# Performance work log

Measured on AMD Instinct MI355X. Metric: run time of the kernel, lower is better.

The kernel has to match this reference:

```python
import jax, jax.numpy as jnp
import numpy as np

B, T, C, H = 4096, 128, 128, 64  # T must equal BLOCK_SIZE=128, C=EMBEDDING_DIM=128


def setup_inputs() -> dict:
    key = jax.random.key(0)
    k1, k2, k3, k4, k5, k6 = jax.random.split(key, 6)
    source_embedding = jax.random.normal(k1, (B, T, C), dtype=jnp.float32)
    target_embedding = jax.random.normal(k2, (B, T, C), dtype=jnp.float32)
    # realistic padding: positions < length are valid; guarantees col 0 valid (no NaN rows)
    lengths = jax.random.randint(k3, (B,), 1, T + 1)
    pad_mask = jnp.arange(T)[None, :] < lengths[:, None]  # (B, T) bool
    Wq = jax.random.normal(k4, (C, H), dtype=jnp.float32) * 0.02
    Wk = jax.random.normal(k5, (C, H), dtype=jnp.float32) * 0.02
    Wv = jax.random.normal(k6, (C, H), dtype=jnp.float32) * 0.02
    return {"source_embedding": source_embedding, "target_embedding": target_embedding,
            "pad_mask": pad_mask, "Wq": Wq, "Wk": Wk, "Wv": Wv}


def reference(source_embedding, target_embedding, pad_mask, Wq, Wk, Wv):
    # q from target, k/v from source (cross-attention capable), bias-free projections
    q = target_embedding @ Wq   # (B, T, H)
    k = source_embedding @ Wk   # (B, T, H)
    v = source_embedding @ Wv   # (B, T, H)
    scale = k.shape[-1] ** -0.5
    wei = jnp.einsum('btd,bsd->bts', q, k) * scale  # (B, T, T)
    causal = jnp.tril(jnp.ones((T, T), dtype=bool))  # needs_future_mask=True
    mask = pad_mask[:, None, :] & causal[None, :, :]  # fuse pad + future masks
    wei = jnp.where(mask, wei, -jnp.inf)
    wei = jax.nn.softmax(wei, axis=-1)
    # dropout disabled (eval mode) for deterministic reference
    out = wei @ v  # (B, T, H)
    return out
```

## Files before the change

### kernel.cpp

```cpp
#include <hip/hip_runtime.h>
#include <stdint.h>


typedef uint32_t u32x2 __attribute__((ext_vector_type(2)));
typedef uint32_t u32x4 __attribute__((ext_vector_type(4)));
typedef float    f32x4 __attribute__((ext_vector_type(4)));
typedef __bf16   bf16x8 __attribute__((ext_vector_type(8)));

static __device__ __forceinline__ uint32_t pack2(float a, float b) {
  uint32_t ua = __builtin_bit_cast(uint32_t, a);
  uint32_t ub = __builtin_bit_cast(uint32_t, b);
  ua += 0x7FFFu + ((ua >> 16) & 1u);
  ub += 0x7FFFu + ((ub >> 16) & 1u);
  return (ua >> 16) | (ub & 0xFFFF0000u);
}
static __device__ __forceinline__ f32x4 mfma16(u32x4 a, u32x4 b, f32x4 c) {
  return __builtin_amdgcn_mfma_f32_16x16x32_bf16(
      __builtin_bit_cast(bf16x8, a), __builtin_bit_cast(bf16x8, b), c, 0, 0, 0);
}

__global__ void prep_w(const float* __restrict__ Wq, const float* __restrict__ Wk,
                       const float* __restrict__ Wv, const void* __restrict__ mask,
                       uint32_t* __restrict__ ws) {
  const int blk = blockIdx.x;
  const int l = threadIdx.x;
  if (blk < 48) {
    const int m  = blk >> 4;
    const int ct = (blk >> 2) & 3;
    const int ks = blk & 3;
    const float* W = (m == 0) ? Wq : ((m == 1) ? Wk : Wv);
    const int h  = ct * 16 + (l & 15);
    const int c0 = ks * 32 + (l >> 4) * 8;
    u32x4 v;
#pragma unroll
    for (int p = 0; p < 4; ++p)
      v[p] = pack2(W[(c0 + 2 * p) * 64 + h], W[(c0 + 2 * p + 1) * 64 + h]);
    ((u32x4*)ws)[blk * 64 + l] = v;
  } else {
    const uint32_t* mw = (const uint32_t*)mask;
    int fl = 0;
    for (int i = l * 16; i < l * 16 + 16; ++i) {
      uint32_t x = mw[i];
      if (x == 0x3F800000u) fl = 2;
      else if (x > 1u && fl != 2) fl = 1;
    }
#pragma unroll
    for (int off = 32; off > 0; off >>= 1) {
      int o = __shfl_down(fl, off);
      fl = (o > fl) ? o : fl;
    }
    if (l == 0) ws[12288] = (uint32_t)fl;
  }
}

__global__ __launch_bounds__(512, 3) void attn_fused(
    const float* __restrict__ src, const float* __restrict__ tgt,
    const void* __restrict__ mask, const uint32_t* __restrict__ ws,
    float* __restrict__ out) {
  __shared__ __align__(16) uint8_t lds[49664];
  uint8_t* const EMB = lds;
  uint8_t* const Kb  = lds + 16384;
  uint8_t* const Vb  = lds + 32768;
  float*  const BIAS = (float*)(lds + 49152);

  const int b   = blockIdx.x;
  const int tid = (int)threadIdx.x;
  const int l   = tid & 63;
  const int w   = tid >> 6;
  const int l15 = l & 15;
  const int g4  = l >> 4;
  const int ct  = w & 3;
  const int sg  = (w >> 2) * 2;

  const u32x4* wsv = (const u32x4*)ws;
  const int mflag = (int)ws[12288];
  const float* const srcb = src + (size_t)b * 16384;
  const float* const tgtb = tgt + (size_t)b * 16384;

  u32x4 wk[4], wv[4];
#pragma unroll
  for (int ks = 0; ks < 4; ++ks) {
    wk[ks] = wsv[((4 + ct) * 4 + ks) * 64 + l];
    wv[ks] = wsv[((8 + ct) * 4 + ks) * 64 + l];
  }

  f32x4 pf[4];
  auto stage_load = [&](const float* gbase) {
#pragma unroll
    for (int p = 0; p < 4; ++p)
      pf[p] = *(const f32x4*)(gbase + tid * 4 + p * 2048);
  };
  auto stage_write = [&]() {
#pragma unroll
    for (int p = 0; p < 4; ++p) {
      const int c   = tid + p * 512;
      const int row = c >> 5;
      const int cc  = c & 31;
      u32x2 d = { pack2(pf[p][0], pf[p][1]), pack2(pf[p][2], pf[p][3]) };
      *(u32x2*)(EMB + (row << 8) + ((((cc >> 1) ^ (row & 7))) << 4) + ((cc & 1) << 3)) = d;
    }
  };

  auto projKV = [&](int half) {
#pragma unroll
    for (int i = 0; i < 2; ++i) {
      const int st  = sg + i;
      const int row = st * 16 + l15;
      f32x4 cK = {0, 0, 0, 0}, cV = {0, 0, 0, 0};
#pragma unroll
      for (int ks = 0; ks < 4; ++ks) {
        u32x4 e = *(const u32x4*)(EMB + (row << 8) + ((((ks * 4 + g4) ^ (row & 7))) << 4));
        cK = mfma16(wk[ks], e, cK);
        cV = mfma16(e, wv[ks], cV);
      }
      const int s  = half * 64 + st * 16 + l15;
      const int h0 = ct * 16 + g4 * 4;
      u32x2 dk = { pack2(cK[0], cK[1]), pack2(cK[2], cK[3]) };
      *(u32x2*)(Kb + (s << 7) + ((((h0 >> 3) ^ (s & 7))) << 4) + ((h0 & 7) << 1)) = dk;
      const int s0 = half * 64 + st * 16 + g4 * 4;
      const int h  = ct * 16 + l15;
      u32x2 dv = { pack2(cV[0], cV[1]), pack2(cV[2], cV[3]) };
      *(u32x2*)(Vb + (h << 8) + ((((s0 >> 3) ^ (h & 7))) << 4) + ((s0 & 7) << 1)) = dv;
    }
  };

  uint32_t qp[8];
  auto projQ_own = [&]() {
    const int row = (w & 3) * 16 + l15;
    f32x4 c0 = {0,0,0,0}, c1 = {0,0,0,0}, c2 = {0,0,0,0}, c3 = {0,0,0,0};
#pragma unroll
    for (int ks = 0; ks < 4; ++ks) {
      u32x4 e = *(const u32x4*)(EMB + (row << 8) + ((((ks * 4 + g4) ^ (row & 7))) << 4));
      c0 = mfma16(wsv[(0  + ks) * 64 + l], e, c0);
      c1 = mfma16(wsv[(4  + ks) * 64 + l], e, c1);
      c2 = mfma16(wsv[(8  + ks) * 64 + l], e, c2);
      c3 = mfma16(wsv[(12 + ks) * 64 + l], e, c3);
    }
    qp[0] = pack2(c0[0], c0[1]); qp[1] = pack2(c0[2], c0[3]);
    qp[2] = pack2(c1[0], c1[1]); qp[3] = pack2(c1[2], c1[3]);
    qp[4] = pack2(c2[0], c2[1]); qp[5] = pack2(c2[2], c2[3]);
    qp[6] = pack2(c3[0], c3[1]); qp[7] = pack2(c3[2], c3[3]);
  };

  stage_load(srcb);
  float biasv = 0.0f;
  if (tid < 128) {
    bool valid;
    if (mflag == 1)      valid = ((const uint8_t*)mask)[b * 128 + tid] != 0;
    else if (mflag == 0) valid = ((const int*)mask)[b * 128 + tid] != 0;
    else                 valid = ((const float*)mask)[b * 128 + tid] != 0.0f;
    biasv = valid ? 0.0f : -1e30f;
  }
  stage_write();
  if (tid < 128) BIAS[tid] = biasv;
  __syncthreads();
  stage_load(srcb + 8192);
  projKV(0);
  __syncthreads();
  stage_write();
  __syncthreads();
  stage_load(tgtb);
  projKV(1);
  __syncthreads();
  stage_write();
  __syncthreads();
  stage_load(tgtb + 8192);
  if (w < 4) projQ_own();
  __syncthreads();
  stage_write();
  __syncthreads();
  if (w >= 4) projQ_own();

  const int hi2 = g4 >> 1;
  const int sA  = ((g4 & 1) * 2) * 16 + l15;
  const int sB  = sA + 16;

  u32x4 qB[2];
#pragma unroll
  for (int ks = 0; ks < 2; ++ks) {
    uint32_t a0 = (uint32_t)__shfl((int)qp[4 * ks + 0], sA);
    uint32_t a1 = (uint32_t)__shfl((int)qp[4 * ks + 1], sA);
    uint32_t a2 = (uint32_t)__shfl((int)qp[4 * ks + 2], sA);
    uint32_t a3 = (uint32_t)__shfl((int)qp[4 * ks + 3], sA);
    uint32_t b0 = (uint32_t)__shfl((int)qp[4 * ks + 0], sB);
    uint32_t b1 = (uint32_t)__shfl((int)qp[4 * ks + 1], sB);
    uint32_t b2 = (uint32_t)__shfl((int)qp[4 * ks + 2], sB);
    uint32_t b3 = (uint32_t)__shfl((int)qp[4 * ks + 3], sB);
    qB[ks][0] = hi2 ? a2 : a0;
    qB[ks][1] = hi2 ? a3 : a1;
    qB[ks][2] = hi2 ? b2 : b0;
    qB[ks][3] = hi2 ? b3 : b1;
  }

  const int tq = 16 * w + l15;
  f32x4 sacc[8];
#pragma unroll
  for (int mt = 0; mt < 8; ++mt) sacc[mt] = {0, 0, 0, 0};
  __builtin_amdgcn_s_setprio(1);
#pragma unroll
  for (int mt = 0; mt < 8; ++mt) {
    const int srow = mt * 16 + l15;
    u32x4 k0 = *(const u32x4*)(Kb + (srow << 7) + (((g4 ^ (srow & 7))) << 4));
    u32x4 k1 = *(const u32x4*)(Kb + (srow << 7) + ((((4 + g4) ^ (srow & 7))) << 4));
    sacc[mt] = mfma16(k0, qB[0], sacc[mt]);
    sacc[mt] = mfma16(k1, qB[1], sacc[mt]);
  }
  __builtin_amdgcn_s_setprio(0);

  float m = -3.0e38f;
#pragma unroll
  for (int mt = 0; mt < 8; ++mt) {
    f32x4 b4 = *(const f32x4*)(BIAS + mt * 16 + g4 * 4);
#pragma unroll
    for (int r = 0; r < 4; ++r) {
      float v = sacc[mt][r] * 0.125f + b4[r];
      sacc[mt][r] = v;
      m = fmaxf(m, v);
    }
  }
  m = fmaxf(m, __shfl_xor(m, 16));
  m = fmaxf(m, __shfl_xor(m, 32));
  float sum = 0.0f;
#pragma unroll
  for (int mt = 0; mt < 8; ++mt) {
#pragma unroll
    for (int r = 0; r < 4; ++r) {
      const int s = mt * 16 + g4 * 4 + r;
      float p = __expf(sacc[mt][r] - m);
      p = (s <= tq) ? p : 0.0f;
      sacc[mt][r] = p;
      sum += p;
    }
  }
  sum += __shfl_xor(sum, 16);
  sum += __shfl_xor(sum, 32);
  const float inv = 1.0f / sum;

  uint32_t sp[16];
#pragma unroll
  for (int mt = 0; mt < 8; ++mt) {
    sp[2 * mt]     = pack2(sacc[mt][0], sacc[mt][1]);
    sp[2 * mt + 1] = pack2(sacc[mt][2], sacc[mt][3]);
  }

  f32x4 oacc[4];
#pragma unroll
  for (int vt = 0; vt < 4; ++vt) oacc[vt] = {0, 0, 0, 0};
  __builtin_amdgcn_s_setprio(1);
#pragma unroll
  for (int ks = 0; ks < 4; ++ks) {
    uint32_t a0 = (uint32_t)__shfl((int)sp[4 * ks + 0], sA);
    uint32_t a1 = (uint32_t)__shfl((int)sp[4 * ks + 1], sA);
    uint32_t a2 = (uint32_t)__shfl((int)sp[4 * ks + 2], sA);
    uint32_t a3 = (uint32_t)__shfl((int)sp[4 * ks + 3], sA);
    uint32_t b0 = (uint32_t)__shfl((int)sp[4 * ks + 0], sB);
    uint32_t b1 = (uint32_t)__shfl((int)sp[4 * ks + 1], sB);
    uint32_t b2 = (uint32_t)__shfl((int)sp[4 * ks + 2], sB);
    uint32_t b3 = (uint32_t)__shfl((int)sp[4 * ks + 3], sB);
    u32x4 pb;
    pb[0] = hi2 ? a2 : a0;
    pb[1] = hi2 ? a3 : a1;
    pb[2] = hi2 ? b2 : b0;
    pb[3] = hi2 ? b3 : b1;
#pragma unroll
    for (int vt = 0; vt < 4; ++vt) {
      const int vrow = vt * 16 + l15;
      u32x4 vf = *(const u32x4*)(Vb + (vrow << 8) + ((((ks * 4 + g4) ^ (vrow & 7))) << 4));
      oacc[vt] = mfma16(vf, pb, oacc[vt]);
    }
  }
  __builtin_amdgcn_s_setprio(0);

  float* const ob = out + (size_t)b * 8192 + (size_t)tq * 64;
#pragma unroll
  for (int vt = 0; vt < 4; ++vt) {
    f32x4 o = { oacc[vt][0] * inv, oacc[vt][1] * inv,
                oacc[vt][2] * inv, oacc[vt][3] * inv };
    *(f32x4*)(ob + vt * 16 + g4 * 4) = o;
  }
}

extern "C" void kernel_launch(void* const* d_in, const int* in_sizes, int n_in,
                              void* d_out, int out_size, void* d_ws, size_t ws_size,
                              hipStream_t stream) {
  const float* src = (const float*)d_in[0];
  const float* tgt = (const float*)d_in[1];
  const void*  msk = d_in[2];
  const float* Wq  = (const float*)d_in[3];
  const float* Wk  = (const float*)d_in[4];
  const float* Wv  = (const float*)d_in[5];
  uint32_t* ws = (uint32_t*)d_ws;
  float* out = (float*)d_out;
  const int B = in_sizes[0] / (128 * 128);

  hipLaunchKernelGGL(prep_w, dim3(49), dim3(64), 0, stream, Wq, Wk, Wv, msk, ws);
  hipLaunchKernelGGL(attn_fused, dim3(B), dim3(512), 0, stream,
                     src, tgt, msk, ws, out);
}
```

Measured before the change: 167.3 us.

## Load embeddings directly from global into MFMA operands, dropping LDS staging

Removes the LDS staging buffer for source/target embeddings. Each wave now reads its fp32 rows straight from global memory into registers, converts them to bf16 and feeds them to the K/V/Q projection MFMAs, which eliminates several staging barriers. The smaller LDS footprint lets the launch bound target four blocks per CU instead of three. Manual bf16 rounding is also replaced by native __bf16 conversion. The trade-off is less coalesced, strided global loads per lane and more register pressure under the tighter occupancy bound.

```diff
diff --git a/kernel.cpp b/kernel.cpp
--- a/kernel.cpp
+++ b/kernel.cpp
@@ -13,6 +13,11 @@
   ua += 0x7FFFu + ((ua >> 16) & 1u);
   ub += 0x7FFFu + ((ub >> 16) & 1u);
   return (ua >> 16) | (ub & 0xFFFF0000u);
+}
+static __device__ __forceinline__ uint32_t cvt2(float a, float b) {
+  uint16_t lo = __builtin_bit_cast(uint16_t, (__bf16)a);
+  uint16_t hi = __builtin_bit_cast(uint16_t, (__bf16)b);
+  return (uint32_t)lo | ((uint32_t)hi << 16);
 }
 static __device__ __forceinline__ f32x4 mfma16(u32x4 a, u32x4 b, f32x4 c) {
   return __builtin_amdgcn_mfma_f32_16x16x32_bf16(
@@ -53,15 +58,14 @@
   }
 }
 
-__global__ __launch_bounds__(512, 3) void attn_fused(
+__global__ __launch_bounds__(512, 4) void attn_fused(
     const float* __restrict__ src, const float* __restrict__ tgt,
     const void* __restrict__ mask, const uint32_t* __restrict__ ws,
     float* __restrict__ out) {
-  __shared__ __align__(16) uint8_t lds[49664];
-  uint8_t* const EMB = lds;
-  uint8_t* const Kb  = lds + 16384;
-  uint8_t* const Vb  = lds + 32768;
-  float*  const BIAS = (float*)(lds + 49152);
+  __shared__ __align__(16) uint8_t lds[33280];
+  uint8_t* const Kb  = lds;
+  uint8_t* const Vb  = lds + 16384;
+  float*  const BIAS = (float*)(lds + 32768);
 
   const int b   = blockIdx.x;
   const int tid = (int)threadIdx.x;
@@ -70,106 +74,76 @@
   const int l15 = l & 15;
   const int g4  = l >> 4;
   const int ct  = w & 3;
-  const int sg  = (w >> 2) * 2;
+  const int sg  = (w >> 2) * 4;
 
   const u32x4* wsv = (const u32x4*)ws;
   const int mflag = (int)ws[12288];
   const float* const srcb = src + (size_t)b * 16384;
   const float* const tgtb = tgt + (size_t)b * 16384;
 
-  u32x4 wk[4], wv[4];
-#pragma unroll
-  for (int ks = 0; ks < 4; ++ks) {
-    wk[ks] = wsv[((4 + ct) * 4 + ks) * 64 + l];
-    wv[ks] = wsv[((8 + ct) * 4 + ks) * 64 + l];
-  }
-
-  f32x4 pf[4];
-  auto stage_load = [&](const float* gbase) {
-#pragma unroll
-    for (int p = 0; p < 4; ++p)
-      pf[p] = *(const f32x4*)(gbase + tid * 4 + p * 2048);
-  };
-  auto stage_write = [&]() {
-#pragma unroll
-    for (int p = 0; p < 4; ++p) {
-      const int c   = tid + p * 512;
-      const int row = c >> 5;
-      const int cc  = c & 31;
-      u32x2 d = { pack2(pf[p][0], pf[p][1]), pack2(pf[p][2], pf[p][3]) };
-      *(u32x2*)(EMB + (row << 8) + ((((cc >> 1) ^ (row & 7))) << 4) + ((cc & 1) << 3)) = d;
-    }
-  };
-
-  auto projKV = [&](int half) {
-#pragma unroll
-    for (int i = 0; i < 2; ++i) {
-      const int st  = sg + i;
-      const int row = st * 16 + l15;
-      f32x4 cK = {0, 0, 0, 0}, cV = {0, 0, 0, 0};
-#pragma unroll
-      for (int ks = 0; ks < 4; ++ks) {
-        u32x4 e = *(const u32x4*)(EMB + (row << 8) + ((((ks * 4 + g4) ^ (row & 7))) << 4));
-        cK = mfma16(wk[ks], e, cK);
-        cV = mfma16(e, wv[ks], cV);
-      }
-      const int s  = half * 64 + st * 16 + l15;
-      const int h0 = ct * 16 + g4 * 4;
-      u32x2 dk = { pack2(cK[0], cK[1]), pack2(cK[2], cK[3]) };
-      *(u32x2*)(Kb + (s << 7) + ((((h0 >> 3) ^ (s & 7))) << 4) + ((h0 & 7) << 1)) = dk;
-      const int s0 = half * 64 + st * 16 + g4 * 4;
-      const int h  = ct * 16 + l15;
-      u32x2 dv = { pack2(cV[0], cV[1]), pack2(cV[2], cV[3]) };
-      *(u32x2*)(Vb + (h << 8) + ((((s0 >> 3) ^ (h & 7))) << 4) + ((s0 & 7) << 1)) = dv;
-    }
-  };
-
-  uint32_t qp[8];
-  auto projQ_own = [&]() {
-    const int row = (w & 3) * 16 + l15;
-    f32x4 c0 = {0,0,0,0}, c1 = {0,0,0,0}, c2 = {0,0,0,0}, c3 = {0,0,0,0};
-#pragma unroll
-    for (int ks = 0; ks < 4; ++ks) {
-      u32x4 e = *(const u32x4*)(EMB + (row << 8) + ((((ks * 4 + g4) ^ (row & 7))) << 4));
-      c0 = mfma16(wsv[(0  + ks) * 64 + l], e, c0);
-      c1 = mfma16(wsv[(4  + ks) * 64 + l], e, c1);
-      c2 = mfma16(wsv[(8  + ks) * 64 + l], e, c2);
-      c3 = mfma16(wsv[(12 + ks) * 64 + l], e, c3);
-    }
-    qp[0] = pack2(c0[0], c0[1]); qp[1] = pack2(c0[2], c0[3]);
-    qp[2] = pack2(c1[0], c1[1]); qp[3] = pack2(c1[2], c1[3]);
-    qp[4] = pack2(c2[0], c2[1]); qp[5] = pack2(c2[2], c2[3]);
-    qp[6] = pack2(c3[0], c3[1]); qp[7] = pack2(c3[2], c3[3]);
-  };
-
-  stage_load(srcb);
-  float biasv = 0.0f;
   if (tid < 128) {
     bool valid;
     if (mflag == 1)      valid = ((const uint8_t*)mask)[b * 128 + tid] != 0;
     else if (mflag == 0) valid = ((const int*)mask)[b * 128 + tid] != 0;
     else                 valid = ((const float*)mask)[b * 128 + tid] != 0.0f;
-    biasv = valid ? 0.0f : -1e30f;
-  }
-  stage_write();
-  if (tid < 128) BIAS[tid] = biasv;
+    BIAS[tid] = valid ? 0.0f : -1e30f;
+  }
+
+  f32x4 cK[4], cV[4];
+#pragma unroll
+  for (int i = 0; i < 4; ++i) { cK[i] = {0,0,0,0}; cV[i] = {0,0,0,0}; }
+#pragma unroll
+  for (int ks = 0; ks < 4; ++ks) {
+    const u32x4 wkf = wsv[((4 + ct) * 4 + ks) * 64 + l];
+    const u32x4 wvf = wsv[((8 + ct) * 4 + ks) * 64 + l];
+#pragma unroll
+    for (int i = 0; i < 4; ++i) {
+      const int row = (sg + i) * 16 + l15;
+      const float* pa = srcb + row * 128 + ks * 32 + g4 * 8;
+      f32x4 a0 = *(const f32x4*)pa;
+      f32x4 a1 = *(const f32x4*)(pa + 4);
+      u32x4 e = { cvt2(a0[0], a0[1]), cvt2(a0[2], a0[3]),
+                  cvt2(a1[0], a1[1]), cvt2(a1[2], a1[3]) };
+      cK[i] = mfma16(wkf, e, cK[i]);
+      cV[i] = mfma16(e, wvf, cV[i]);
+    }
+  }
+#pragma unroll
+  for (int i = 0; i < 4; ++i) {
+    const int st = sg + i;
+    const int s  = st * 16 + l15;
+    const int h0 = ct * 16 + g4 * 4;
+    u32x2 dk = { cvt2(cK[i][0], cK[i][1]), cvt2(cK[i][2], cK[i][3]) };
+    *(u32x2*)(Kb + (s << 7) + ((((h0 >> 3) ^ (s & 7))) << 4) + ((h0 & 7) << 1)) = dk;
+    const int s0 = st * 16 + g4 * 4;
+    const int h  = ct * 16 + l15;
+    u32x2 dv = { cvt2(cV[i][0], cV[i][1]), cvt2(cV[i][2], cV[i][3]) };
+    *(u32x2*)(Vb + (h << 8) + ((((s0 >> 3) ^ (h & 7))) << 4) + ((s0 & 7) << 1)) = dv;
+  }
+
+  uint32_t qp[8];
+  {
+    const float* pq = tgtb + (16 * w + l15) * 128;
+    f32x4 c0 = {0,0,0,0}, c1 = {0,0,0,0}, c2 = {0,0,0,0}, c3 = {0,0,0,0};
+#pragma unroll
+    for (int ks = 0; ks < 4; ++ks) {
+      const float* pa = pq + ks * 32 + g4 * 8;
+      f32x4 a0 = *(const f32x4*)pa;
+      f32x4 a1 = *(const f32x4*)(pa + 4);
+      u32x4 e = { cvt2(a0[0], a0[1]), cvt2(a0[2], a0[3]),
+                  cvt2(a1[0], a1[1]), cvt2(a1[2], a1[3]) };
+      c0 = mfma16(wsv[(0  + ks) * 64 + l], e, c0);
+      c1 = mfma16(wsv[(4  + ks) * 64 + l], e, c1);
+      c2 = mfma16(wsv[(8  + ks) * 64 + l], e, c2);
+      c3 = mfma16(wsv[(12 + ks) * 64 + l], e, c3);
+    }
+    qp[0] = cvt2(c0[0], c0[1]); qp[1] = cvt2(c0[2], c0[3]);
+    qp[2] = cvt2(c1[0], c1[1]); qp[3] = cvt2(c1[2], c1[3]);
+    qp[4] = cvt2(c2[0], c2[1]); qp[5] = cvt2(c2[2], c2[3]);
+    qp[6] = cvt2(c3[0], c3[1]); qp[7] = cvt2(c3[2], c3[3]);
+  }
+
   __syncthreads();
-  stage_load(srcb + 8192);
-  projKV(0);
-  __syncthreads();
-  stage_write();
-  __syncthreads();
-  stage_load(tgtb);
-  projKV(1);
-  __syncthreads();
-  stage_write();
-  __syncthreads();
-  stage_load(tgtb + 8192);
-  if (w < 4) projQ_own();
-  __syncthreads();
-  stage_write();
-  __syncthreads();
-  if (w >= 4) projQ_own();
 
   const int hi2 = g4 >> 1;
   const int sA  = ((g4 & 1) * 2) * 16 + l15;
@@ -239,8 +213,8 @@
   uint32_t sp[16];
 #pragma unroll
   for (int mt = 0; mt < 8; ++mt) {
-    sp[2 * mt]     = pack2(sacc[mt][0], sacc[mt][1]);
-    sp[2 * mt + 1] = pack2(sacc[mt][2], sacc[mt][3]);
+    sp[2 * mt]     = cvt2(sacc[mt][0], sacc[mt][1]);
+    sp[2 * mt + 1] = cvt2(sacc[mt][2], sacc[mt][3]);
   }
 
   f32x4 oacc[4];
```

After: 217.4 us. 29.9% more time.

## Load Q embeddings straight from global into registers and use hardware bf16 conversion

Applied to the files above, without the earlier changes.

Each wave now reads its own 16 target rows directly from global memory into registers and computes the Q projection up front, rather than staging the target embedding through LDS in two halves. This removes two stage/sync rounds and the matching LDS writes and reads. The manual round-to-nearest bf16 packing is also replaced with the compiler's __bf16 cast, which can map to a hardware convert instruction. The cost is more live registers held across the K/V phase, plus global reads that are less coalesced per lane.

```diff
diff --git a/kernel.cpp b/kernel.cpp
--- a/kernel.cpp
+++ b/kernel.cpp
@@ -13,6 +13,11 @@
   ua += 0x7FFFu + ((ua >> 16) & 1u);
   ub += 0x7FFFu + ((ub >> 16) & 1u);
   return (ua >> 16) | (ub & 0xFFFF0000u);
+}
+static __device__ __forceinline__ uint32_t cvt2(float a, float b) {
+  uint16_t lo = __builtin_bit_cast(uint16_t, (__bf16)a);
+  uint16_t hi = __builtin_bit_cast(uint16_t, (__bf16)b);
+  return (uint32_t)lo | ((uint32_t)hi << 16);
 }
 static __device__ __forceinline__ f32x4 mfma16(u32x4 a, u32x4 b, f32x4 c) {
   return __builtin_amdgcn_mfma_f32_16x16x32_bf16(
@@ -71,77 +76,28 @@
   const int g4  = l >> 4;
   const int ct  = w & 3;
   const int sg  = (w >> 2) * 2;
+  const int tq  = 16 * w + l15;
 
   const u32x4* wsv = (const u32x4*)ws;
   const int mflag = (int)ws[12288];
   const float* const srcb = src + (size_t)b * 16384;
   const float* const tgtb = tgt + (size_t)b * 16384;
 
-  u32x4 wk[4], wv[4];
-#pragma unroll
-  for (int ks = 0; ks < 4; ++ks) {
-    wk[ks] = wsv[((4 + ct) * 4 + ks) * 64 + l];
-    wv[ks] = wsv[((8 + ct) * 4 + ks) * 64 + l];
-  }
-
+  f32x4 qv[8];
+  {
+    const float* pq = tgtb + tq * 128 + g4 * 8;
+#pragma unroll
+    for (int ks = 0; ks < 4; ++ks) {
+      qv[2 * ks]     = *(const f32x4*)(pq + ks * 32);
+      qv[2 * ks + 1] = *(const f32x4*)(pq + ks * 32 + 4);
+    }
+  }
   f32x4 pf[4];
   auto stage_load = [&](const float* gbase) {
 #pragma unroll
     for (int p = 0; p < 4; ++p)
       pf[p] = *(const f32x4*)(gbase + tid * 4 + p * 2048);
   };
-  auto stage_write = [&]() {
-#pragma unroll
-    for (int p = 0; p < 4; ++p) {
-      const int c   = tid + p * 512;
-      const int row = c >> 5;
-      const int cc  = c & 31;
-      u32x2 d = { pack2(pf[p][0], pf[p][1]), pack2(pf[p][2], pf[p][3]) };
-      *(u32x2*)(EMB + (row << 8) + ((((cc >> 1) ^ (row & 7))) << 4) + ((cc & 1) << 3)) = d;
-    }
-  };
-
-  auto projKV = [&](int half) {
-#pragma unroll
-    for (int i = 0; i < 2; ++i) {
-      const int st  = sg + i;
-      const int row = st * 16 + l15;
-      f32x4 cK = {0, 0, 0, 0}, cV = {0, 0, 0, 0};
-#pragma unroll
-      for (int ks = 0; ks < 4; ++ks) {
-        u32x4 e = *(const u32x4*)(EMB + (row << 8) + ((((ks * 4 + g4) ^ (row & 7))) << 4));
-        cK = mfma16(wk[ks], e, cK);
-        cV = mfma16(e, wv[ks], cV);
-      }
-      const int s  = half * 64 + st * 16 + l15;
-      const int h0 = ct * 16 + g4 * 4;
-      u32x2 dk = { pack2(cK[0], cK[1]), pack2(cK[2], cK[3]) };
-      *(u32x2*)(Kb + (s << 7) + ((((h0 >> 3) ^ (s & 7))) << 4) + ((h0 & 7) << 1)) = dk;
-      const int s0 = half * 64 + st * 16 + g4 * 4;
-      const int h  = ct * 16 + l15;
-      u32x2 dv = { pack2(cV[0], cV[1]), pack2(cV[2], cV[3]) };
-      *(u32x2*)(Vb + (h << 8) + ((((s0 >> 3) ^ (h & 7))) << 4) + ((s0 & 7) << 1)) = dv;
-    }
-  };
-
-  uint32_t qp[8];
-  auto projQ_own = [&]() {
-    const int row = (w & 3) * 16 + l15;
-    f32x4 c0 = {0,0,0,0}, c1 = {0,0,0,0}, c2 = {0,0,0,0}, c3 = {0,0,0,0};
-#pragma unroll
-    for (int ks = 0; ks < 4; ++ks) {
-      u32x4 e = *(const u32x4*)(EMB + (row << 8) + ((((ks * 4 + g4) ^ (row & 7))) << 4));
-      c0 = mfma16(wsv[(0  + ks) * 64 + l], e, c0);
-      c1 = mfma16(wsv[(4  + ks) * 64 + l], e, c1);
-      c2 = mfma16(wsv[(8  + ks) * 64 + l], e, c2);
-      c3 = mfma16(wsv[(12 + ks) * 64 + l], e, c3);
-    }
-    qp[0] = pack2(c0[0], c0[1]); qp[1] = pack2(c0[2], c0[3]);
-    qp[2] = pack2(c1[0], c1[1]); qp[3] = pack2(c1[2], c1[3]);
-    qp[4] = pack2(c2[0], c2[1]); qp[5] = pack2(c2[2], c2[3]);
-    qp[6] = pack2(c3[0], c3[1]); qp[7] = pack2(c3[2], c3[3]);
-  };
-
   stage_load(srcb);
   float biasv = 0.0f;
   if (tid < 128) {
@@ -151,6 +107,64 @@
     else                 valid = ((const float*)mask)[b * 128 + tid] != 0.0f;
     biasv = valid ? 0.0f : -1e30f;
   }
+
+  uint32_t qp[8];
+  {
+    f32x4 c0 = {0,0,0,0}, c1 = {0,0,0,0}, c2 = {0,0,0,0}, c3 = {0,0,0,0};
+#pragma unroll
+    for (int ks = 0; ks < 4; ++ks) {
+      u32x4 e = { cvt2(qv[2*ks][0], qv[2*ks][1]), cvt2(qv[2*ks][2], qv[2*ks][3]),
+                  cvt2(qv[2*ks+1][0], qv[2*ks+1][1]), cvt2(qv[2*ks+1][2], qv[2*ks+1][3]) };
+      c0 = mfma16(wsv[(0  + ks) * 64 + l], e, c0);
+      c1 = mfma16(wsv[(4  + ks) * 64 + l], e, c1);
+      c2 = mfma16(wsv[(8  + ks) * 64 + l], e, c2);
+      c3 = mfma16(wsv[(12 + ks) * 64 + l], e, c3);
+    }
+    qp[0] = cvt2(c0[0], c0[1]); qp[1] = cvt2(c0[2], c0[3]);
+    qp[2] = cvt2(c1[0], c1[1]); qp[3] = cvt2(c1[2], c1[3]);
+    qp[4] = cvt2(c2[0], c2[1]); qp[5] = cvt2(c2[2], c2[3]);
+    qp[6] = cvt2(c3[0], c3[1]); qp[7] = cvt2(c3[2], c3[3]);
+  }
+
+  auto stage_write = [&]() {
+#pragma unroll
+    for (int p = 0; p < 4; ++p) {
+      const int c   = tid + p * 512;
+      const int row = c >> 5;
+      const int cc  = c & 31;
+      u32x2 d = { cvt2(pf[p][0], pf[p][1]), cvt2(pf[p][2], pf[p][3]) };
+      *(u32x2*)(EMB + (row << 8) + ((((cc >> 1) ^ (row & 7))) << 4) + ((cc & 1) << 3)) = d;
+    }
+  };
+  u32x4 wk[4], wv[4];
+#pragma unroll
+  for (int ks = 0; ks < 4; ++ks) {
+    wk[ks] = wsv[((4 + ct) * 4 + ks) * 64 + l];
+    wv[ks] = wsv[((8 + ct) * 4 + ks) * 64 + l];
+  }
+  auto projKV = [&](int half) {
+#pragma unroll
+    for (int i = 0; i < 2; ++i) {
+      const int st  = sg + i;
+      const int row = st * 16 + l15;
+      f32x4 cK = {0, 0, 0, 0}, cV = {0, 0, 0, 0};
+#pragma unroll
+      for (int ks = 0; ks < 4; ++ks) {
+        u32x4 e = *(const u32x4*)(EMB + (row << 8) + ((((ks * 4 + g4) ^ (row & 7))) << 4));
+        cK = mfma16(wk[ks], e, cK);
+        cV = mfma16(e, wv[ks], cV);
+      }
+      const int s  = half * 64 + st * 16 + l15;
+      const int h0 = ct * 16 + g4 * 4;
+      u32x2 dk = { cvt2(cK[0], cK[1]), cvt2(cK[2], cK[3]) };
+      *(u32x2*)(Kb + (s << 7) + ((((h0 >> 3) ^ (s & 7))) << 4) + ((h0 & 7) << 1)) = dk;
+      const int s0 = half * 64 + st * 16 + g4 * 4;
+      const int h  = ct * 16 + l15;
+      u32x2 dv = { cvt2(cV[0], cV[1]), cvt2(cV[2], cV[3]) };
+      *(u32x2*)(Vb + (h << 8) + ((((s0 >> 3) ^ (h & 7))) << 4) + ((s0 & 7) << 1)) = dv;
+    }
+  };
+
   stage_write();
   if (tid < 128) BIAS[tid] = biasv;
   __syncthreads();
@@ -159,17 +173,8 @@
   __syncthreads();
   stage_write();
   __syncthreads();
-  stage_load(tgtb);
   projKV(1);
   __syncthreads();
-  stage_write();
-  __syncthreads();
-  stage_load(tgtb + 8192);
-  if (w < 4) projQ_own();
-  __syncthreads();
-  stage_write();
-  __syncthreads();
-  if (w >= 4) projQ_own();
 
   const int hi2 = g4 >> 1;
   const int sA  = ((g4 & 1) * 2) * 16 + l15;
@@ -192,7 +197,6 @@
     qB[ks][3] = hi2 ? b3 : b1;
   }
 
-  const int tq = 16 * w + l15;
   f32x4 sacc[8];
 #pragma unroll
   for (int mt = 0; mt < 8; ++mt) sacc[mt] = {0, 0, 0, 0};
@@ -239,8 +243,8 @@
   uint32_t sp[16];
 #pragma unroll
   for (int mt = 0; mt < 8; ++mt) {
-    sp[2 * mt]     = pack2(sacc[mt][0], sacc[mt][1]);
-    sp[2 * mt + 1] = pack2(sacc[mt][2], sacc[mt][3]);
+    sp[2 * mt]     = cvt2(sacc[mt][0], sacc[mt][1]);
+    sp[2 * mt + 1] = cvt2(sacc[mt][2], sacc[mt][3]);
   }
 
   f32x4 oacc[4];
```

After: 154.1 us. 7.9% less time.
